# Kernel optimization log

Measured on AMD Instinct MI355X. Metric: run time of the kernel, lower is better.

The kernel has to match this reference:

```python
import jax, jax.numpy as jnp
import numpy as np

B, L, D, H, K_DELAYS = 8, 2048, 512, 8, 8
DH = D // H


def setup_inputs() -> dict:
    key = jax.random.key(0)
    ks = jax.random.split(key, 6)
    def lin_w(k):
        return 0.02 * jax.random.normal(k, (D, D), jnp.float32)
    return {
        "x_q":  jax.random.normal(ks[0], (B, L, D), jnp.float32),
        "x_kv": jax.random.normal(ks[1], (B, L, D), jnp.float32),
        "Wq": lin_w(ks[2]), "bq": jnp.zeros((D,), jnp.float32),
        "Wk": lin_w(ks[3]), "bk": jnp.zeros((D,), jnp.float32),
        "Wv": lin_w(ks[4]), "bv": jnp.zeros((D,), jnp.float32),
        "Wo": lin_w(ks[5]), "bo": jnp.zeros((D,), jnp.float32),
    }


def reference(x_q, x_kv, Wq, bq, Wk, bk, Wv, bv, Wo, bo):
    Bx, Lx, Dx = x_q.shape

    def proj(x, W, b):  # torch Linear: x @ W.T + b, then split heads -> [B,H,L,dh]
        return (x @ W.T + b).reshape(Bx, Lx, H, DH).transpose(0, 2, 1, 3)

    q = proj(x_q, Wq, bq)
    k = proj(x_kv, Wk, bk)
    v = proj(x_kv, Wv, bv)

    # FFT-based autocorrelation over the time axis (axis=2)
    qz = q - q.mean(axis=2, keepdims=True)
    kz = k - k.mean(axis=2, keepdims=True)
    Qf = jnp.fft.rfft(qz, axis=2)
    Kf = jnp.fft.rfft(kz, axis=2)
    corr = jnp.fft.irfft(Qf * jnp.conj(Kf), n=Lx, axis=2).mean(axis=-1)  # [B,H,L]
    # torch expands corr to [B,H,Lq,Lk] then means over Lq -> identical to corr
    score = corr

    K = min(K_DELAYS, Lx)
    vals, idx = jax.lax.top_k(score, K)                    # [B,H,K]
    w = vals / (vals.sum(axis=-1, keepdims=True) + 1e-12)
    w = jax.lax.stop_gradient(w)                           # .detach() in torch

    # circular shift by -delay == gather at (t + delay) mod L
    t = jnp.arange(Lx)
    pos = (t[None, None, None, :] + idx[..., None]) % Lx   # [B,H,K,L]
    v_sh = jnp.take_along_axis(v[:, :, None, :, :], pos[..., None], axis=3)  # [B,H,K,L,dh]
    out = jnp.einsum('bhk,bhkld->bhld', w, v_sh)           # weighted sum over delays

    out = out.transpose(0, 2, 1, 3).reshape(Bx, Lx, Dx)
    return out @ Wo.T + bo
```

## Files before the change

### kernel.cpp

```cpp
#include <hip/hip_runtime.h>
#include <math.h>

#define BB 8
#define LL 2048
#define DD 512
#define HH 8
#define DHH 64
#define KD 8
#define MM (BB*LL)

typedef _Float16 f16x4 __attribute__((ext_vector_type(4)));
typedef _Float16 f16x8 __attribute__((ext_vector_type(8)));
typedef float    f32x4 __attribute__((ext_vector_type(4)));

__device__ inline void cvt8(const float* __restrict__ s, _Float16* hp, _Float16* lp) {
    const float4 a = *(const float4*)s;
    const float4 b = *(const float4*)(s + 4);
    const float v[8] = {a.x, a.y, a.z, a.w, b.x, b.y, b.z, b.w};
    f16x8 hi, lo;
#pragma unroll
    for (int j = 0; j < 8; j++) {
        const _Float16 h = (_Float16)v[j];
        hi[j] = h;
        lo[j] = (_Float16)((v[j] - (float)h) * 512.0f);
    }
    *(f16x8*)hp = hi;
    if (lp) *(f16x8*)lp = lo;
}

__global__ __launch_bounds__(256) void prep_all(const float* __restrict__ xq,
                                                const float* __restrict__ xkv,
                                                const float* __restrict__ Wq, const float* __restrict__ Wk,
                                                const float* __restrict__ Wv, const float* __restrict__ Wo,
                                                _Float16* __restrict__ Xq_h, _Float16* __restrict__ Xq_l,
                                                _Float16* __restrict__ Xkv_h, _Float16* __restrict__ Xkv_l,
                                                _Float16* __restrict__ Wq_h, _Float16* __restrict__ Wq_l,
                                                _Float16* __restrict__ Wk_h, _Float16* __restrict__ Wk_l,
                                                _Float16* __restrict__ Wv_h, _Float16* __restrict__ Wo_h) {
    const int bid = blockIdx.x;
    if (bid < 8192) {
        const int g = bid * 256 + threadIdx.x;
        const int which = g >> 20;
        const size_t idx = (size_t)(g & 1048575) * 8;
        const float* src = which ? xkv : xq;
        _Float16* dh = which ? Xkv_h : Xq_h;
        _Float16* dl = which ? Xkv_l : Xq_l;
        cvt8(src + idx, dh + idx, dl + idx);
    } else {
        const int g = (bid - 8192) * 256 + threadIdx.x;
        const int which = g >> 15;
        const size_t idx = (size_t)(g & 32767) * 8;
        if (which == 0)      cvt8(Wq + idx, Wq_h + idx, Wq_l + idx);
        else if (which == 1) cvt8(Wk + idx, Wk_h + idx, Wk_l + idx);
        else if (which == 2) cvt8(Wv + idx, Wv_h + idx, nullptr);
        else                 cvt8(Wo + idx, Wo_h + idx, nullptr);
    }
}

template<int NPROD, int MODE>
__device__ __forceinline__ void gemm_body(const _Float16* __restrict__ Ag,
                                          const _Float16* __restrict__ Al_g,
                                          const _Float16* __restrict__ Bg,
                                          const _Float16* __restrict__ Bl_g,
                                          const float* __restrict__ bias,
                                          void* __restrict__ Cv,
                                          _Float16* lds, int l0) {
    _Float16* Ah = lds;
    _Float16* Bh = lds + 5120;
    _Float16* Al = (NPROD == 3) ? lds + 10240 : lds;
    _Float16* Bl = (NPROD == 3) ? lds + 15360 : lds;

    const int t  = threadIdx.x;
    const int m0 = (((l0 >> 5) << 3) | (l0 & 7)) * 128;
    const int n0 = ((l0 >> 3) & 3) * 128;

    const int lrow = t >> 2;
    const int lcol = (t & 3) * 8;
    const int wave = t >> 6;
    const int lane = t & 63;
    const int wm   = (wave >> 1) * 64;
    const int wn   = (wave & 1) * 64;
    const int lm   = lane & 15;
    const int quad = lane >> 4;

    f32x4 acc0[4][4] = {};
    f32x4 acc1[4][4] = {};

    f16x8 pa[2], pb[2], pal[2], pbl[2];
#pragma unroll
    for (int p = 0; p < 2; p++) {
        pa[p] = *(const f16x8*)(Ag + (size_t)(m0 + p * 64 + lrow) * 512 + lcol);
        pb[p] = *(const f16x8*)(Bg + (size_t)(n0 + p * 64 + lrow) * 512 + lcol);
        if (NPROD == 3) {
            pal[p] = *(const f16x8*)(Al_g + (size_t)(m0 + p * 64 + lrow) * 512 + lcol);
            pbl[p] = *(const f16x8*)(Bl_g + (size_t)(n0 + p * 64 + lrow) * 512 + lcol);
        }
    }

    for (int k0 = 0; k0 < 512; k0 += 32) {
        __syncthreads();
#pragma unroll
        for (int p = 0; p < 2; p++) {
            const int row = p * 64 + lrow;
            *(f16x8*)&Ah[row * 40 + lcol] = pa[p];
            *(f16x8*)&Bh[row * 40 + lcol] = pb[p];
            if (NPROD == 3) {
                *(f16x8*)&Al[row * 40 + lcol] = pal[p];
                *(f16x8*)&Bl[row * 40 + lcol] = pbl[p];
            }
        }
        __syncthreads();

        if (k0 + 32 < 512) {
            const int kn = k0 + 32;
#pragma unroll
            for (int p = 0; p < 2; p++) {
                pa[p] = *(const f16x8*)(Ag + (size_t)(m0 + p * 64 + lrow) * 512 + kn + lcol);
                pb[p] = *(const f16x8*)(Bg + (size_t)(n0 + p * 64 + lrow) * 512 + kn + lcol);
                if (NPROD == 3) {
                    pal[p] = *(const f16x8*)(Al_g + (size_t)(m0 + p * 64 + lrow) * 512 + kn + lcol);
                    pbl[p] = *(const f16x8*)(Bl_g + (size_t)(n0 + p * 64 + lrow) * 512 + kn + lcol);
                }
            }
        }

        f16x8 afh[4], bf[4];
#pragma unroll
        for (int mt = 0; mt < 4; mt++)
            afh[mt] = *(f16x8*)&Ah[(wm + mt * 16 + lm) * 40 + quad * 8];
#pragma unroll
        for (int nt = 0; nt < 4; nt++)
            bf[nt] = *(f16x8*)&Bh[(wn + nt * 16 + lm) * 40 + quad * 8];

#pragma unroll
        for (int mt = 0; mt < 4; mt++)
#pragma unroll
            for (int nt = 0; nt < 4; nt++)
                acc0[mt][nt] = __builtin_amdgcn_mfma_f32_16x16x32_f16(afh[mt], bf[nt], acc0[mt][nt], 0, 0, 0);

        if (NPROD == 3) {
            f16x8 afl[4];
#pragma unroll
            for (int mt = 0; mt < 4; mt++)
                afl[mt] = *(f16x8*)&Al[(wm + mt * 16 + lm) * 40 + quad * 8];
#pragma unroll
            for (int mt = 0; mt < 4; mt++)
#pragma unroll
                for (int nt = 0; nt < 4; nt++)
                    acc1[mt][nt] = __builtin_amdgcn_mfma_f32_16x16x32_f16(afl[mt], bf[nt], acc1[mt][nt], 0, 0, 0);
#pragma unroll
            for (int nt = 0; nt < 4; nt++)
                bf[nt] = *(f16x8*)&Bl[(wn + nt * 16 + lm) * 40 + quad * 8];
#pragma unroll
            for (int mt = 0; mt < 4; mt++)
#pragma unroll
                for (int nt = 0; nt < 4; nt++)
                    acc1[mt][nt] = __builtin_amdgcn_mfma_f32_16x16x32_f16(afh[mt], bf[nt], acc1[mt][nt], 0, 0, 0);
        }
    }

#pragma unroll
    for (int mt = 0; mt < 4; mt++) {
#pragma unroll
        for (int nt = 0; nt < 4; nt++) {
            const int n = n0 + wn + nt * 16 + lm;
            const float bv = bias[n];
            float val[4];
#pragma unroll
            for (int r = 0; r < 4; r++) {
                val[r] = acc0[mt][nt][r] + bv;
                if (NPROD == 3) val[r] += acc1[mt][nt][r] * (1.0f / 512.0f);
            }
            const int mbase = m0 + wm + mt * 16 + quad * 4;
            const int b_idx = mbase >> 11;
            const int lbase = mbase & 2047;
            if (MODE == 0) {
                float* C = (float*)Cv;
#pragma unroll
                for (int r = 0; r < 4; r++) C[(size_t)(mbase + r) * 512 + n] = val[r];
            } else if (MODE == 1) {
                float* C = (float*)Cv;
                float4 pv = make_float4(val[0], val[1], val[2], val[3]);
                *(float4*)&C[((size_t)(b_idx * 512 + n)) * 2048 + lbase] = pv;
            } else {
                _Float16* C = (_Float16*)Cv;
#pragma unroll
                for (int r = 0; r < 4; r++)
                    C[(size_t)b_idx * 1048576 + (size_t)(n >> 6) * 131072
                      + (size_t)(lbase + r) * 64 + (n & 63)] = (_Float16)val[r];
            }
        }
    }
}

__global__ __launch_bounds__(256, 2) void gemm_qk(const _Float16* __restrict__ A0h, const _Float16* __restrict__ A0l,
                                                  const _Float16* __restrict__ B0h, const _Float16* __restrict__ B0l,
                                                  const float* __restrict__ bias0, float* __restrict__ C0,
                                                  const _Float16* __restrict__ A1h, const _Float16* __restrict__ A1l,
                                                  const _Float16* __restrict__ B1h, const _Float16* __restrict__ B1l,
                                                  const float* __restrict__ bias1, float* __restrict__ C1) {
    __shared__ __align__(16) _Float16 lds[20480];
    const int prob = blockIdx.x >> 9;
    const int l0   = blockIdx.x & 511;
    if (prob == 0)
        gemm_body<3, 1>(A0h, A0l, B0h, B0l, bias0, C0, lds, l0);
    else
        gemm_body<3, 1>(A1h, A1l, B1h, B1l, bias1, C1, lds, l0);
}

__global__ __launch_bounds__(256, 2) void gemm_v(const _Float16* __restrict__ Ah_g,
                                                 const _Float16* __restrict__ Bh_g,
                                                 const float* __restrict__ bias,
                                                 _Float16* __restrict__ C) {
    __shared__ __align__(16) _Float16 lds[10240];
    gemm_body<1, 2>(Ah_g, Ah_g, Bh_g, Bh_g, bias, C, lds, blockIdx.x);
}

__global__ __launch_bounds__(256, 2) void gemm_o(const _Float16* __restrict__ Ah_g,
                                                 const _Float16* __restrict__ Bh_g,
                                                 const float* __restrict__ bias,
                                                 float* __restrict__ C) {
    __shared__ __align__(16) _Float16 lds[10240];
    gemm_body<1, 0>(Ah_g, Ah_g, Bh_g, Bh_g, bias, C, lds, blockIdx.x);
}

#define PAD3(i) ((i) + ((i) >> 3))

__device__ inline float2 cmul2(float2 a, float2 w) {
    return make_float2(a.x * w.x - a.y * w.y, a.x * w.y + a.y * w.x);
}
__device__ inline float2 cadd2(float2 a, float2 b) { return make_float2(a.x + b.x, a.y + b.y); }
__device__ inline float2 csub2(float2 a, float2 b) { return make_float2(a.x - b.x, a.y - b.y); }

__global__ __launch_bounds__(256) void fft_fwd(const float* __restrict__ qT,
                                               const float* __restrict__ kT,
                                               float* __restrict__ specP) {
    const int blk  = blockIdx.x;
    const int bh   = blk >> 4;
    const int part = blk & 15;
    const int t    = threadIdx.x;
    __shared__ float2 Zs[2304];
    __shared__ float2 Wt[1024];

#pragma unroll
    for (int s = 0; s < 4; s++) {
        const int j = t + s * 256;
        float sv, cv;
        __sincosf(2.0f * (float)M_PI * (float)j / 2048.0f, &sv, &cv);
        Wt[j] = make_float2(cv, -sv);
    }

    float2 pacc[8];
#pragma unroll
    for (int s = 0; s < 8; s++) pacc[s] = make_float2(0.0f, 0.0f);

    const int low5 = t & 31, hi3 = t >> 5;
    const int low2 = t & 3,  hi6 = t >> 2;

    for (int j4 = 0; j4 < 4; j4++) {
        const int seq = bh * 64 + part * 4 + j4;
        const float* qp = qT + (size_t)seq * 2048;
        const float* kp = kT + (size_t)seq * 2048;
        float2 z[8];
#pragma unroll
        for (int s = 0; s < 8; s++) z[s] = make_float2(qp[t + 256 * s], kp[t + 256 * s]);
        __syncthreads();

#pragma unroll
        for (int sp = 0; sp < 4; sp++) {
            float2 u = z[sp], v = z[sp + 4];
            z[sp]     = cadd2(u, v);
            z[sp + 4] = cmul2(csub2(u, v), Wt[t + 256 * sp]);
        }
#pragma unroll
        for (int base = 0; base < 8; base += 4)
#pragma unroll
            for (int q2 = 0; q2 < 2; q2++) {
                float2 u = z[base + q2], v = z[base + q2 + 2];
                z[base + q2]     = cadd2(u, v);
                z[base + q2 + 2] = cmul2(csub2(u, v), Wt[2 * (t + 256 * q2)]);
            }
        {
            const float2 w = Wt[4 * t];
#pragma unroll
            for (int e = 0; e < 8; e += 2) {
                float2 u = z[e], v = z[e + 1];
                z[e]     = cadd2(u, v);
                z[e + 1] = cmul2(csub2(u, v), w);
            }
        }

#pragma unroll
        for (int s = 0; s < 8; s++) Zs[PAD3(t + 256 * s)] = z[s];
        __syncthreads();
#pragma unroll
        for (int s = 0; s < 8; s++) z[s] = Zs[PAD3(low5 + 32 * s + 256 * hi3)];

#pragma unroll
        for (int sp = 0; sp < 4; sp++) {
            float2 u = z[sp], v = z[sp + 4];
            z[sp]     = cadd2(u, v);
            z[sp + 4] = cmul2(csub2(u, v), Wt[8 * (low5 + 32 * sp)]);
        }
#pragma unroll
        for (int base = 0; base < 8; base += 4)
#pragma unroll
            for (int q2 = 0; q2 < 2; q2++) {
                float2 u = z[base + q2], v = z[base + q2 + 2];
                z[base + q2]     = cadd2(u, v);
                z[base + q2 + 2] = cmul2(csub2(u, v), Wt[16 * (low5 + 32 * q2)]);
            }
        {
            const float2 w = Wt[32 * low5];
#pragma unroll
            for (int e = 0; e < 8; e += 2) {
                float2 u = z[e], v = z[e + 1];
                z[e]     = cadd2(u, v);
                z[e + 1] = cmul2(csub2(u, v), w);
            }
        }

#pragma unroll
        for (int s = 0; s < 8; s++) Zs[PAD3(low5 + 32 * s + 256 * hi3)] = z[s];
        __syncthreads();
#pragma unroll
        for (int s = 0; s < 8; s++) z[s] = Zs[PAD3(low2 + 4 * s + 32 * hi6)];

#pragma unroll
        for (int sp = 0; sp < 4; sp++) {
            float2 u = z[sp], v = z[sp + 4];
            z[sp]     = cadd2(u, v);
            z[sp + 4] = cmul2(csub2(u, v), Wt[64 * (low2 + 4 * sp)]);
        }
#pragma unroll
        for (int base = 0; base < 8; base += 4)
#pragma unroll
            for (int q2 = 0; q2 < 2; q2++) {
                float2 u = z[base + q2], v = z[base + q2 + 2];
                z[base + q2]     = cadd2(u, v);
                z[base + q2 + 2] = cmul2(csub2(u, v), Wt[128 * (low2 + 4 * q2)]);
            }
        {
            const float2 w = Wt[256 * low2];
#pragma unroll
            for (int e = 0; e < 8; e += 2) {
                float2 u = z[e], v = z[e + 1];
                z[e]     = cadd2(u, v);
                z[e + 1] = cmul2(csub2(u, v), w);
            }
        }

#pragma unroll
        for (int s = 0; s < 8; s++) Zs[PAD3(low2 + 4 * s + 32 * hi6)] = z[s];
        __syncthreads();
#pragma unroll
        for (int s = 0; s < 8; s++) z[s] = Zs[PAD3(8 * t + s)];

#pragma unroll
        for (int base = 0; base < 8; base += 4) {
            {
                float2 u = z[base], v = z[base + 2];
                z[base]     = cadd2(u, v);
                z[base + 2] = csub2(u, v);
            }
            {
                float2 u = z[base + 1], v = z[base + 3];
                float2 d = csub2(u, v);
                z[base + 1] = cadd2(u, v);
                z[base + 3] = make_float2(d.y, -d.x);
            }
        }
#pragma unroll
        for (int e = 0; e < 8; e += 2) {
            float2 u = z[e], v = z[e + 1];
            z[e]     = cadd2(u, v);
            z[e + 1] = csub2(u, v);
        }

#pragma unroll
        for (int s = 0; s < 8; s++) Zs[PAD3(8 * t + s)] = z[s];
        __syncthreads();

#pragma unroll
        for (int s = 0; s < 8; s++) {
            const int p  = t + 256 * s;
            const int f  = (int)(__brev((unsigned)p) >> 21);
            const int fm = (2048 - f) & 2047;
            const int p2 = (int)(__brev((unsigned)fm) >> 21);
            const float2 zf = Zs[PAD3(p)];
            const float2 zm = Zs[PAD3(p2)];
            const float qr = 0.5f * (zf.x + zm.x);
            const float qi = 0.5f * (zf.y - zm.y);
            const float kr = 0.5f * (zf.y + zm.y);
            const float ki = 0.5f * (zm.x - zf.x);
            if (f != 0) {
                pacc[s].x += qr * kr + qi * ki;
                pacc[s].y += qi * kr - qr * ki;
            }
        }
    }

    float2* outp = (float2*)specP + (size_t)blk * 2048;
#pragma unroll
    for (int s = 0; s < 8; s++) outp[t + 256 * s] = pacc[s];
}

__device__ inline void build_twiddle(float2* Wt, int tid, float sign) {
#pragma unroll
    for (int s = 0; s < 4; s++) {
        const int j = tid + s * 256;
        const float a = 2.0f * (float)M_PI * (float)j / 2048.0f;
        float sv, cv;
        __sincosf(a, &sv, &cv);
        Wt[j] = make_float2(cv, sign * sv);
    }
}

__device__ inline void fft2048_stages(float2* Z, const float2* Wt, int tid) {
    for (int st = 0; st < 11; st++) {
        const int half = 1 << st;
        const int shift = 10 - st;
#pragma unroll
        for (int r = 0; r < 4; r++) {
            const int m   = tid + r * 256;
            const int grp = m >> st;
            const int pos = m & (half - 1);
            const int i0  = (grp << (st + 1)) + pos;
            const int i1  = i0 + half;
            const float2 w = Wt[pos << shift];
            const float2 a = Z[i0];
            const float2 b = Z[i1];
            const float tr = b.x * w.x - b.y * w.y;
            const float ti = b.x * w.y + b.y * w.x;
            Z[i0] = make_float2(a.x + tr, a.y + ti);
            Z[i1] = make_float2(a.x - tr, a.y - ti);
        }
        __syncthreads();
    }
}

__global__ __launch_bounds__(256) void fft_inv_topk(const float* __restrict__ specP,
                                                    int* __restrict__ delays,
                                                    float* __restrict__ weights) {
    const int bh  = blockIdx.x;
    const int tid = threadIdx.x;
    __shared__ float2 Z[2048];
    __shared__ float2 Wt[1024];
    __shared__ float  corrS[2048];
    __shared__ float  rv[256];
    __shared__ int    ri[256];
    __shared__ float  vals[KD];
    __shared__ int    inds[KD];

    build_twiddle(Wt, tid, +1.0f);

    const float2* sp = (const float2*)specP + (size_t)bh * 16 * 2048;
#pragma unroll
    for (int s = 0; s < 8; s++) {
        const int p = tid + s * 256;
        float2 acc = make_float2(0.0f, 0.0f);
#pragma unroll
        for (int part = 0; part < 16; part++) {
            const float2 v = sp[part * 2048 + p];
            acc.x += v.x; acc.y += v.y;
        }
        Z[p] = acc;
    }
    __syncthreads();
    fft2048_stages(Z, Wt, tid);

    const float scale = 1.0f / (2048.0f * 64.0f);
#pragma unroll
    for (int s = 0; s < 8; s++) {
        const int i = tid + s * 256;
        corrS[i] = Z[i].x * scale;
    }
    __syncthreads();

    for (int k = 0; k < KD; k++) {
        float best = -1e30f;
        int   bi   = 1 << 30;
        for (int i = tid; i < 2048; i += 256) {
            const float v = corrS[i];
            if (v > best || (v == best && i < bi)) { best = v; bi = i; }
        }
        rv[tid] = best;
        ri[tid] = bi;
        __syncthreads();
        for (int off = 128; off > 0; off >>= 1) {
            if (tid < off) {
                const float v2 = rv[tid + off];
                const int   i2 = ri[tid + off];
                if (v2 > rv[tid] || (v2 == rv[tid] && i2 < ri[tid])) {
                    rv[tid] = v2; ri[tid] = i2;
                }
            }
            __syncthreads();
        }
        if (tid == 0) {
            vals[k] = rv[0];
            inds[k] = ri[0];
            corrS[ri[0]] = -1e30f;
        }
        __syncthreads();
    }

    if (tid == 0) {
        float sum = 0.0f;
        for (int k = 0; k < KD; k++) sum += vals[k];
        const float inv = 1.0f / (sum + 1e-12f);
        for (int k = 0; k < KD; k++) {
            weights[bh * KD + k] = vals[k] * inv;
            delays[bh * KD + k]  = inds[k];
        }
    }
}

__global__ __launch_bounds__(256) void gather_ws(const _Float16* __restrict__ v,
                                                 const int* __restrict__ delays,
                                                 const float* __restrict__ weights,
                                                 _Float16* __restrict__ outb) {
    const int gp = blockIdx.x * 256 + threadIdx.x;
    const int c8 = gp & 63;
    const int m  = gp >> 6;
    const int l  = m & 2047;
    const int b  = m >> 11;
    const int ch = c8 * 8;
    const int h  = ch >> 6;
    const int dh = ch & 63;
    const int bh = b * 8 + h;

    const _Float16* vb = v + (size_t)bh * 131072;
    float a[8] = {};
#pragma unroll
    for (int k = 0; k < KD; k++) {
        const int   d = delays[bh * KD + k];
        const float w = weights[bh * KD + k];
        const int   p = (l + d) & 2047;
        const f16x8 pv = *(const f16x8*)&vb[p * 64 + dh];
#pragma unroll
        for (int j = 0; j < 8; j++) a[j] = fmaf(w, (float)pv[j], a[j]);
    }
    f16x8 ov;
#pragma unroll
    for (int j = 0; j < 8; j++) ov[j] = (_Float16)a[j];
    *(f16x8*)&outb[(size_t)m * 512 + ch] = ov;
}

extern "C" void kernel_launch(void* const* d_in, const int* in_sizes, int n_in,
                              void* d_out, int out_size, void* d_ws, size_t ws_size,
                              hipStream_t stream) {
    const float* x_q  = (const float*)d_in[0];
    const float* x_kv = (const float*)d_in[1];
    const float* Wq   = (const float*)d_in[2];
    const float* bq   = (const float*)d_in[3];
    const float* Wk   = (const float*)d_in[4];
    const float* bk   = (const float*)d_in[5];
    const float* Wv   = (const float*)d_in[6];
    const float* bv   = (const float*)d_in[7];
    const float* Wo   = (const float*)d_in[8];
    const float* bo   = (const float*)d_in[9];
    float* out = (float*)d_out;

    char* ws = (char*)d_ws;
    _Float16* Xq_h  = (_Float16*)(ws + 0);
    _Float16* Xq_l  = (_Float16*)(ws + 16777216);
    _Float16* Xkv_h = (_Float16*)(ws + 33554432);
    _Float16* Xkv_l = (_Float16*)(ws + 50331648);
    _Float16* Wq_h  = (_Float16*)(ws + 67108864);
    _Float16* Wq_l  = (_Float16*)(ws + 67633152);
    _Float16* Wk_h  = (_Float16*)(ws + 68157440);
    _Float16* Wk_l  = (_Float16*)(ws + 68681728);
    _Float16* Wv_h  = (_Float16*)(ws + 69206016);
    _Float16* Wo_h  = (_Float16*)(ws + 69730304);
    int*      dely  = (int*)    (ws + 70254592);
    float*    wgt   = (float*)  (ws + 70256640);
    float*    kf32  = (float*)  (ws + 75497472);
    float*    specP = (float*)  (ws + 113246208);
    _Float16* vh    = (_Float16*)(ws + 130023424);
    _Float16* gbuf  = (_Float16*)(ws + 146800640);
    float*    qf32  = (float*)d_out;

    dim3 blk(256);

    prep_all<<<dim3(8704), blk, 0, stream>>>(x_q, x_kv, Wq, Wk, Wv, Wo,
                                             Xq_h, Xq_l, Xkv_h, Xkv_l,
                                             Wq_h, Wq_l, Wk_h, Wk_l, Wv_h, Wo_h);

    gemm_qk<<<dim3(1024), blk, 0, stream>>>(Xq_h,  Xq_l,  Wq_h, Wq_l, bq, qf32,
                                            Xkv_h, Xkv_l, Wk_h, Wk_l, bk, kf32);

    fft_fwd<<<dim3(1024), blk, 0, stream>>>(qf32, kf32, specP);

    fft_inv_topk<<<dim3(BB * HH), blk, 0, stream>>>(specP, dely, wgt);

    gemm_v<<<dim3(512), blk, 0, stream>>>(Xkv_h, Wv_h, bv, vh);

    gather_ws<<<dim3(4096), blk, 0, stream>>>(vh, dely, wgt, gbuf);

    gemm_o<<<dim3(512), blk, 0, stream>>>(gbuf, Wo_h, bo, out);
}
```

Before: 300.7 us.

## Stage GEMM tiles with direct global-to-LDS loads and double-buffer single-product GEMMs

Replaces the register-staged global→LDS copy in the shared GEMM body with `__builtin_amdgcn_global_load_lds` direct loads. Each wave fills one operand region of the padded 40-half row layout; the pad segment is filled by re-loading a valid segment. For the single-product V and O GEMMs it adds a two-buffer LDS ping-pong, so the next K tile loads while MFMAs run on the current one, doubling their LDS allocation. The split QK GEMM keeps a single buffer but still skips the register round trip. The risks are about 20% redundant load traffic from the pad segments, lower occupancy from the larger LDS footprint, and dependence on barriers waiting for the async LDS writes.

```diff
diff --git a/kernel.cpp b/kernel.cpp
--- a/kernel.cpp
+++ b/kernel.cpp
@@ -57,6 +57,50 @@
     }
 }
 
+template<int NPROD>
+__device__ __forceinline__ void mfma_step(const _Float16* cb,
+                                          int wm, int wn, int lm, int quad,
+                                          f32x4 (&acc0)[4][4], f32x4 (&acc1)[4][4]) {
+    const _Float16* Ah = cb;
+    const _Float16* Bh = cb + 5120;
+    const _Float16* Al = cb + 10240;
+    const _Float16* Bl = cb + 15360;
+
+    f16x8 afh[4], bf[4];
+#pragma unroll
+    for (int mt = 0; mt < 4; mt++)
+        afh[mt] = *(const f16x8*)&Ah[(wm + mt * 16 + lm) * 40 + quad * 8];
+#pragma unroll
+    for (int nt = 0; nt < 4; nt++)
+        bf[nt] = *(const f16x8*)&Bh[(wn + nt * 16 + lm) * 40 + quad * 8];
+
+#pragma unroll
+    for (int mt = 0; mt < 4; mt++)
+#pragma unroll
+        for (int nt = 0; nt < 4; nt++)
+            acc0[mt][nt] = __builtin_amdgcn_mfma_f32_16x16x32_f16(afh[mt], bf[nt], acc0[mt][nt], 0, 0, 0);
+
+    if (NPROD == 3) {
+        f16x8 afl[4];
+#pragma unroll
+        for (int mt = 0; mt < 4; mt++)
+            afl[mt] = *(const f16x8*)&Al[(wm + mt * 16 + lm) * 40 + quad * 8];
+#pragma unroll
+        for (int mt = 0; mt < 4; mt++)
+#pragma unroll
+            for (int nt = 0; nt < 4; nt++)
+                acc1[mt][nt] = __builtin_amdgcn_mfma_f32_16x16x32_f16(afl[mt], bf[nt], acc1[mt][nt], 0, 0, 0);
+#pragma unroll
+        for (int nt = 0; nt < 4; nt++)
+            bf[nt] = *(const f16x8*)&Bl[(wn + nt * 16 + lm) * 40 + quad * 8];
+#pragma unroll
+        for (int mt = 0; mt < 4; mt++)
+#pragma unroll
+            for (int nt = 0; nt < 4; nt++)
+                acc1[mt][nt] = __builtin_amdgcn_mfma_f32_16x16x32_f16(afh[mt], bf[nt], acc1[mt][nt], 0, 0, 0);
+    }
+}
+
 template<int NPROD, int MODE>
 __device__ __forceinline__ void gemm_body(const _Float16* __restrict__ Ag,
                                           const _Float16* __restrict__ Al_g,
@@ -65,17 +109,10 @@
                                           const float* __restrict__ bias,
                                           void* __restrict__ Cv,
                                           _Float16* lds, int l0) {
-    _Float16* Ah = lds;
-    _Float16* Bh = lds + 5120;
-    _Float16* Al = (NPROD == 3) ? lds + 10240 : lds;
-    _Float16* Bl = (NPROD == 3) ? lds + 15360 : lds;
-
     const int t  = threadIdx.x;
     const int m0 = (((l0 >> 5) << 3) | (l0 & 7)) * 128;
     const int n0 = ((l0 >> 3) & 3) * 128;
 
-    const int lrow = t >> 2;
-    const int lcol = (t & 3) * 8;
     const int wave = t >> 6;
     const int lane = t & 63;
     const int wm   = (wave >> 1) * 64;
@@ -86,76 +123,51 @@
     f32x4 acc0[4][4] = {};
     f32x4 acc1[4][4] = {};
 
-    f16x8 pa[2], pb[2], pal[2], pbl[2];
-#pragma unroll
-    for (int p = 0; p < 2; p++) {
-        pa[p] = *(const f16x8*)(Ag + (size_t)(m0 + p * 64 + lrow) * 512 + lcol);
-        pb[p] = *(const f16x8*)(Bg + (size_t)(n0 + p * 64 + lrow) * 512 + lcol);
-        if (NPROD == 3) {
-            pal[p] = *(const f16x8*)(Al_g + (size_t)(m0 + p * 64 + lrow) * 512 + lcol);
-            pbl[p] = *(const f16x8*)(Bl_g + (size_t)(n0 + p * 64 + lrow) * 512 + lcol);
-        }
-    }
-
-    for (int k0 = 0; k0 < 512; k0 += 32) {
-        __syncthreads();
-#pragma unroll
-        for (int p = 0; p < 2; p++) {
-            const int row = p * 64 + lrow;
-            *(f16x8*)&Ah[row * 40 + lcol] = pa[p];
-            *(f16x8*)&Bh[row * 40 + lcol] = pb[p];
-            if (NPROD == 3) {
-                *(f16x8*)&Al[row * 40 + lcol] = pal[p];
-                *(f16x8*)&Bl[row * 40 + lcol] = pbl[p];
-            }
-        }
-        __syncthreads();
-
-        if (k0 + 32 < 512) {
-            const int kn = k0 + 32;
-#pragma unroll
-            for (int p = 0; p < 2; p++) {
-                pa[p] = *(const f16x8*)(Ag + (size_t)(m0 + p * 64 + lrow) * 512 + kn + lcol);
-                pb[p] = *(const f16x8*)(Bg + (size_t)(n0 + p * 64 + lrow) * 512 + kn + lcol);
-                if (NPROD == 3) {
-                    pal[p] = *(const f16x8*)(Al_g + (size_t)(m0 + p * 64 + lrow) * 512 + kn + lcol);
-                    pbl[p] = *(const f16x8*)(Bl_g + (size_t)(n0 + p * 64 + lrow) * 512 + kn + lcol);
-                }
-            }
-        }
-
-        f16x8 afh[4], bf[4];
-#pragma unroll
-        for (int mt = 0; mt < 4; mt++)
-            afh[mt] = *(f16x8*)&Ah[(wm + mt * 16 + lm) * 40 + quad * 8];
-#pragma unroll
-        for (int nt = 0; nt < 4; nt++)
-            bf[nt] = *(f16x8*)&Bh[(wn + nt * 16 + lm) * 40 + quad * 8];
-
-#pragma unroll
-        for (int mt = 0; mt < 4; mt++)
-#pragma unroll
-            for (int nt = 0; nt < 4; nt++)
-                acc0[mt][nt] = __builtin_amdgcn_mfma_f32_16x16x32_f16(afh[mt], bf[nt], acc0[mt][nt], 0, 0, 0);
-
-        if (NPROD == 3) {
-            f16x8 afl[4];
-#pragma unroll
-            for (int mt = 0; mt < 4; mt++)
-                afl[mt] = *(f16x8*)&Al[(wm + mt * 16 + lm) * 40 + quad * 8];
-#pragma unroll
-            for (int mt = 0; mt < 4; mt++)
-#pragma unroll
-                for (int nt = 0; nt < 4; nt++)
-                    acc1[mt][nt] = __builtin_amdgcn_mfma_f32_16x16x32_f16(afl[mt], bf[nt], acc1[mt][nt], 0, 0, 0);
-#pragma unroll
-            for (int nt = 0; nt < 4; nt++)
-                bf[nt] = *(f16x8*)&Bl[(wn + nt * 16 + lm) * 40 + quad * 8];
-#pragma unroll
-            for (int mt = 0; mt < 4; mt++)
-#pragma unroll
-                for (int nt = 0; nt < 4; nt++)
-                    acc1[mt][nt] = __builtin_amdgcn_mfma_f32_16x16x32_f16(afh[mt], bf[nt], acc1[mt][nt], 0, 0, 0);
+    const _Float16* sbase;
+    int srow0, soff, segbase;
+    if (NPROD == 3) {
+        sbase   = (wave == 0) ? Ag : (wave == 1) ? Bg : (wave == 2) ? Al_g : Bl_g;
+        srow0   = (wave & 1) ? n0 : m0;
+        soff    = wave * 5120;
+        segbase = 0;
+    } else {
+        sbase   = (wave < 2) ? Ag : Bg;
+        srow0   = (wave < 2) ? m0 : n0;
+        soff    = (wave < 2) ? 0 : 5120;
+        segbase = (wave & 1) * 320;
+    }
+    constexpr int NJ = (NPROD == 3) ? 10 : 5;
+
+    auto stage = [&](_Float16* buf, int kk) {
+#pragma unroll
+        for (int j = 0; j < NJ; j++) {
+            const int seg = segbase + j * 64 + lane;
+            const int r   = seg / 5;
+            int s = seg - r * 5;
+            if (s == 4) s = 3;
+            const _Float16* gp = sbase + (size_t)(srow0 + r) * 512 + kk + s * 8;
+            __builtin_amdgcn_global_load_lds(
+                (const __attribute__((address_space(1))) unsigned int*)gp,
+                (__attribute__((address_space(3))) unsigned int*)(buf + soff + (segbase + j * 64) * 8),
+                16, 0, 0);
+        }
+    };
+
+    if (NPROD == 3) {
+        for (int k0 = 0; k0 < 512; k0 += 32) {
+            __syncthreads();
+            stage(lds, k0);
+            __syncthreads();
+            mfma_step<NPROD>(lds, wm, wn, lm, quad, acc0, acc1);
+        }
+    } else {
+        stage(lds, 0);
+        int p = 0;
+        for (int k0 = 0; k0 < 512; k0 += 32) {
+            __syncthreads();
+            if (k0 + 32 < 512) stage(p ? lds : lds + 10240, k0 + 32);
+            mfma_step<NPROD>(p ? lds + 10240 : lds, wm, wn, lm, quad, acc0, acc1);
+            p ^= 1;
         }
     }
 
@@ -212,7 +224,7 @@
                                                  const _Float16* __restrict__ Bh_g,
                                                  const float* __restrict__ bias,
                                                  _Float16* __restrict__ C) {
-    __shared__ __align__(16) _Float16 lds[10240];
+    __shared__ __align__(16) _Float16 lds[20480];
     gemm_body<1, 2>(Ah_g, Ah_g, Bh_g, Bh_g, bias, C, lds, blockIdx.x);
 }
 
@@ -220,7 +232,7 @@
                                                  const _Float16* __restrict__ Bh_g,
                                                  const float* __restrict__ bias,
                                                  float* __restrict__ C) {
-    __shared__ __align__(16) _Float16 lds[10240];
+    __shared__ __align__(16) _Float16 lds[20480];
     gemm_body<1, 0>(Ah_g, Ah_g, Bh_g, Bh_g, bias, C, lds, blockIdx.x);
 }
 
```

Measured after the change: 301.4 us. No clear change (+0.2%).
